# Optimization experiments

Measured on AMD Instinct MI355X. Metric: run time of the kernel, lower is better.

The kernel has to match this reference:

```python
import jax, jax.numpy as jnp
import numpy as np

D_MODEL = 1024
NUM_HEADS = 16
SEQ_LEN = 2048
BATCH = 2
THETA = 10000.0


def apply_rope(x, positions, theta=THETA):
    # x: [b, h, s, d]; positions: [s] int
    d = x.shape[-1]
    inv_freq = 1.0 / (theta ** (jnp.arange(0, d, 2, dtype=jnp.float32) / d))  # [d/2]
    ang = positions.astype(jnp.float32)[:, None] * inv_freq[None, :]  # [s, d/2]
    cos, sin = jnp.cos(ang), jnp.sin(ang)  # [s, d/2]
    x_even = x[..., 0::2]
    x_odd = x[..., 1::2]
    out_even = x_even * cos - x_odd * sin
    out_odd = x_even * sin + x_odd * cos
    # re-interleave pairs
    out = jnp.stack([out_even, out_odd], axis=-1).reshape(x.shape)
    return out


def setup_inputs() -> dict:
    key = jax.random.key(0)
    ks = jax.random.split(key, 5)
    scale = 1.0 / np.sqrt(D_MODEL)
    return {
        "in_features": jax.random.normal(ks[0], (BATCH, SEQ_LEN, D_MODEL), dtype=jnp.float32),
        "token_positions": jnp.arange(SEQ_LEN, dtype=jnp.int32),
        "q_w": jax.random.normal(ks[1], (D_MODEL, D_MODEL), dtype=jnp.float32) * scale,
        "k_w": jax.random.normal(ks[2], (D_MODEL, D_MODEL), dtype=jnp.float32) * scale,
        "v_w": jax.random.normal(ks[3], (D_MODEL, D_MODEL), dtype=jnp.float32) * scale,
        "o_w": jax.random.normal(ks[4], (D_MODEL, D_MODEL), dtype=jnp.float32) * scale,
    }


def reference(in_features, token_positions, q_w, k_w, v_w, o_w):
    b, s, _ = in_features.shape
    h = NUM_HEADS
    d_k = D_MODEL // h

    # Linear stores weights [out, in]: y = x @ W^T
    def proj(x, w):
        y = jnp.einsum('bsi,oi->bso', x, w)
        return y.reshape(b, s, h, d_k).transpose(0, 2, 1, 3)  # [b, h, s, d]

    q = apply_rope(proj(in_features, q_w), token_positions)
    k = apply_rope(proj(in_features, k_w), token_positions)
    v = proj(in_features, v_w)

    scores = jnp.einsum('bhqd,bhkd->bhqk', q, k) / jnp.sqrt(jnp.float32(d_k))
    causal = jnp.tril(jnp.ones((s, s), dtype=bool))
    scores = jnp.where(causal, scores, jnp.float32(-1e30))
    attn = jax.nn.softmax(scores, axis=-1)
    out = jnp.einsum('bhqk,bhkd->bhqd', attn, v)  # [b, h, s, d]
    out = out.transpose(0, 2, 1, 3).reshape(b, s, h * d_k)
    return jnp.einsum('bsi,oi->bso', out, o_w)
```

## Files before the change

kernel.cpp:

```cpp
#include <hip/hip_runtime.h>
#include <hip/hip_bf16.h>

typedef unsigned short ushort_t;
typedef unsigned int uint_t;
typedef __attribute__((ext_vector_type(4))) float f32x4;
typedef __attribute__((ext_vector_type(16))) float f32x16;
typedef __attribute__((ext_vector_type(8))) short short8;
typedef __attribute__((ext_vector_type(4))) short short4x;
typedef __attribute__((ext_vector_type(4))) unsigned short u16x4;
typedef __attribute__((ext_vector_type(2))) uint_t u32x2;

typedef const __attribute__((address_space(1))) unsigned char glob_t;
typedef __attribute__((address_space(3))) unsigned char lds_t;

#define S_LEN 2048
#define DM 1024
#define NH 16
#define DH 64
#define NB 2
#define BH (NB*NH)
#define MROWS (NB*S_LEN)

#define SCALE_L2E 0.18033688f

__device__ __forceinline__ float bf2f(ushort_t u) {
    return __uint_as_float(((uint_t)u) << 16);
}
__device__ __forceinline__ ushort_t f2bf(float f) {
    __hip_bfloat16 h = __float2bfloat16(f);
    return *reinterpret_cast<ushort_t*>(&h);
}

__global__ __launch_bounds__(256) void convert_all(
    const float* __restrict__ X,  const float* __restrict__ Wq,
    const float* __restrict__ Wk, const float* __restrict__ Wv,
    const float* __restrict__ Wo,
    ushort_t* __restrict__ Xb,  ushort_t* __restrict__ Wqb,
    ushort_t* __restrict__ Wkb, ushort_t* __restrict__ Wvb,
    ushort_t* __restrict__ Wob)
{
    size_t i = (size_t)blockIdx.x * 256 + threadIdx.x;
    size_t e = i * 4;
    const float* src; ushort_t* dst; size_t off;
    if (e < (size_t)MROWS * DM) { src = X; dst = Xb; off = e; }
    else {
        size_t r = e - (size_t)MROWS * DM;
        int w = (int)(r >> 20); off = r & 1048575;
        src = (w == 0) ? Wq : (w == 1) ? Wk : (w == 2) ? Wv : Wo;
        dst = (w == 0) ? Wqb : (w == 1) ? Wkb : (w == 2) ? Wvb : Wob;
    }
    float4 v = *reinterpret_cast<const float4*>(src + off);
    u16x4 o;
    o[0] = f2bf(v.x); o[1] = f2bf(v.y); o[2] = f2bf(v.z); o[3] = f2bf(v.w);
    *reinterpret_cast<u16x4*>(dst + off) = o;
}

__global__ __launch_bounds__(256) void rope_table_k(
    const int* __restrict__ pos, float2* __restrict__ tab)
{
    int i = blockIdx.x * 256 + threadIdx.x;
    int s = i >> 5, f = i & 31;
    float inv = powf(10000.0f, -(float)f / 32.0f);
    float ang = (float)pos[s] * inv;
    tab[i] = make_float2(cosf(ang), sinf(ang));
}

template<int MODE>
__global__ __launch_bounds__(256) void gemm128b(
    const ushort_t* __restrict__ A,
    const ushort_t* __restrict__ W0, const ushort_t* __restrict__ W1,
    const ushort_t* __restrict__ W2,
    ushort_t* __restrict__ D0, ushort_t* __restrict__ D1,
    ushort_t* __restrict__ D2,
    float* __restrict__ Fout, const float2* __restrict__ tab)
{
    __shared__ __attribute__((aligned(16))) ushort_t As[128 * 32];
    __shared__ __attribute__((aligned(16))) ushort_t Bs[128 * 32];
    const ushort_t* W = (MODE == 1 || blockIdx.z == 0) ? W0
                        : (blockIdx.z == 1 ? W1 : W2);
    ushort_t* Dst = (blockIdx.z == 0) ? D0 : (blockIdx.z == 1) ? D1 : D2;
    int m0 = blockIdx.x * 128, n0 = blockIdx.y * 128;
    int tid = threadIdx.x, lane = tid & 63, wv = tid >> 6;
    int wm = wv >> 1, wn = wv & 1;
    int l15 = lane & 15, g = lane >> 4;

    f32x4 acc[4][4];
    for (int i = 0; i < 4; i++)
        for (int j = 0; j < 4; j++)
            acc[i][j] = (f32x4){0.f, 0.f, 0.f, 0.f};

    int srow = wv * 32 + (lane >> 2);
    int scol = (lane & 3) * 8;
    const ushort_t* Ap = A + (size_t)(m0 + srow) * DM + scol;
    const ushort_t* Wp = W + (size_t)(n0 + srow) * DM + scol;
    lds_t* laA0 = (lds_t*)&As[wv * 1024];
    lds_t* laA1 = (lds_t*)&As[wv * 1024 + 512];
    lds_t* laB0 = (lds_t*)&Bs[wv * 1024];
    lds_t* laB1 = (lds_t*)&Bs[wv * 1024 + 512];

    for (int kk = 0; kk < DM; kk += 32) {
        __builtin_amdgcn_global_load_lds((glob_t*)(Ap + kk), laA0, 16, 0, 0);
        __builtin_amdgcn_global_load_lds((glob_t*)(Ap + 16 * DM + kk), laA1, 16, 0, 0);
        __builtin_amdgcn_global_load_lds((glob_t*)(Wp + kk), laB0, 16, 0, 0);
        __builtin_amdgcn_global_load_lds((glob_t*)(Wp + 16 * DM + kk), laB1, 16, 0, 0);
        __syncthreads();
        short8 af[4], bf[4];
        for (int i = 0; i < 4; i++)
            af[i] = *reinterpret_cast<const short8*>(
                &As[(wm * 64 + i * 16 + l15) * 32 + g * 8]);
        for (int j = 0; j < 4; j++)
            bf[j] = *reinterpret_cast<const short8*>(
                &Bs[(wn * 64 + j * 16 + l15) * 32 + g * 8]);
        __builtin_amdgcn_s_setprio(1);
        for (int i = 0; i < 4; i++)
            for (int j = 0; j < 4; j++)
                acc[i][j] = __builtin_amdgcn_mfma_f32_16x16x32_bf16(
                    af[i], bf[j], acc[i][j], 0, 0, 0);
        __builtin_amdgcn_s_setprio(0);
        __syncthreads();
    }

    for (int i = 0; i < 4; i++) {
        for (int j = 0; j < 4; j++) {
            int mbase = m0 + wm * 64 + i * 16 + g * 4;
            int n = n0 + wn * 64 + j * 16 + l15;
            if (MODE == 0) {
                int h = n >> 6, d = n & 63;
                if (blockIdx.z < 2) {
                    int f = d >> 1;
                    float sgn = (d & 1) ? 1.f : -1.f;
                    float sc = (blockIdx.z == 0) ? SCALE_L2E : 1.0f;
                    for (int r = 0; r < 4; r++) {
                        int m = mbase + r;
                        int b = m >> 11, s = m & 2047;
                        float v = acc[i][j][r];
                        float p = __shfl_xor(v, 1);
                        float2 cs = tab[s * 32 + f];
                        float out = (v * cs.x + p * cs.y * sgn) * sc;
                        Dst[(((size_t)(b * NH + h)) * S_LEN + s) * DH + d] =
                            f2bf(out);
                    }
                } else {
                    for (int r = 0; r < 4; r++) {
                        int m = mbase + r;
                        int b = m >> 11, s = m & 2047;
                        Dst[((size_t)(b * NH + h) * DH + d) * S_LEN + s] =
                            f2bf(acc[i][j][r]);
                    }
                }
            } else {
                for (int r = 0; r < 4; r++)
                    Fout[(size_t)(mbase + r) * DM + n] = acc[i][j][r];
            }
        }
    }
}

__global__ __launch_bounds__(256, 2) void attn_k6(
    const ushort_t* __restrict__ Q, const ushort_t* __restrict__ K,
    const ushort_t* __restrict__ Vt, ushort_t* __restrict__ O)
{
    __shared__ __attribute__((aligned(16))) ushort_t Ks[2][4096];
    __shared__ __attribute__((aligned(16))) ushort_t Vs[2][4096];

    int tid = threadIdx.x, wv = tid >> 6, lane = tid & 63;
    int l31 = lane & 31, h = lane >> 5, r7 = l31 & 7;
    int bid = blockIdx.x;
    int grp = bid >> 5;
    int u = (bid < 256) ? (15 - grp) : (grp - 8);
    int bh = bid & 31;
    int qb0 = u * 128;
    int qmin = qb0 + wv * 32, qmax = qmin + 31;
    int nt = 2 * u + 2;

    const ushort_t* Qp = Q + (size_t)bh * S_LEN * DH;
    const char* Kp = (const char*)(K + (size_t)bh * S_LEN * DH);
    const char* Vp = (const char*)(Vt + (size_t)bh * DH * S_LEN);

    short8 qf[4];
    {
        const ushort_t* qp = Qp + (((size_t)(qmin + l31)) << 6) + h * 8;
        #pragma unroll
        for (int ds = 0; ds < 4; ds++)
            qf[ds] = *reinterpret_cast<const short8*>(qp + ds * 16);
    }

    f32x16 oacc[2];
    oacc[0] = (f32x16){0.f};
    oacc[1] = (f32x16){0.f};
    float m_run = -INFINITY, l_run = 0.f;

#define STAGE6(buf, kk0) do {                                                 \
    _Pragma("unroll") for (int c_ = 0; c_ < 2; ++c_) {                        \
        int L_ = c_ * 4096 + wv * 1024 + lane * 16;                           \
        int row_ = L_ >> 7;                                                   \
        int col_ = (L_ & 127) ^ ((row_ & 7) << 4);                            \
        __builtin_amdgcn_global_load_lds(                                     \
            (glob_t*)(Kp + (size_t)((kk0) + row_) * 128 + col_),              \
            (lds_t*)((char*)&Ks[buf][0] + c_ * 4096 + wv * 1024), 16, 0, 0);  \
        __builtin_amdgcn_global_load_lds(                                     \
            (glob_t*)(Vp + (size_t)row_ * (S_LEN * 2) + (size_t)(kk0) * 2     \
                      + col_),                                                \
            (lds_t*)((char*)&Vs[buf][0] + c_ * 4096 + wv * 1024), 16, 0, 0);  \
    } } while (0)

    STAGE6(0, 0);
    __syncthreads();

    int cur = 0;
    for (int t = 0; t < nt; ++t) {
        int k0 = t << 6;
        if (t + 1 < nt) STAGE6(cur ^ 1, (t + 1) << 6);

        if (k0 <= qmax) {
            const char* kb = (const char*)&Ks[cur][0];
            const char* vbp = (const char*)&Vs[cur][0];
            short8 kf[2][4];
            #pragma unroll
            for (int s = 0; s < 2; s++)
                #pragma unroll
                for (int ds = 0; ds < 4; ds++)
                    kf[s][ds] = *reinterpret_cast<const short8*>(
                        kb + (s * 32 + l31) * 128 + (((h + 2 * ds) ^ r7) << 4));
            short4x vb[2][2][4];
            #pragma unroll
            for (int ss = 0; ss < 2; ss++)
                #pragma unroll
                for (int db = 0; db < 2; db++)
                    #pragma unroll
                    for (int kt = 0; kt < 4; kt++)
                        vb[ss][db][kt] = *reinterpret_cast<const short4x*>(
                            vbp + (db * 32 + l31) * 128
                            + ((((ss << 2) + kt) ^ r7) << 4) + h * 8);

            f32x16 st[2];
            __builtin_amdgcn_s_setprio(1);
            #pragma unroll
            for (int s = 0; s < 2; s++) {
                f32x16 z = {0.f};
                #pragma unroll
                for (int ds = 0; ds < 4; ds++)
                    z = __builtin_amdgcn_mfma_f32_32x32x16_bf16(
                        kf[s][ds], qf[ds], z, 0, 0, 0);
                st[s] = z;
            }
            __builtin_amdgcn_s_setprio(0);

            if (k0 + 63 > qmin) {
                int q = qmin + l31;
                #pragma unroll
                for (int s = 0; s < 2; s++)
                    #pragma unroll
                    for (int r = 0; r < 16; r++)
                        if ((k0 + s * 32 + (r & 3) + 8 * (r >> 2) + 4 * h) > q)
                            st[s][r] = -1e30f;
            }

            float m0v = fmaxf(st[0][0], st[0][1]);
            #pragma unroll
            for (int r = 2; r < 16; r++) m0v = fmaxf(m0v, st[0][r]);
            float m1v = fmaxf(st[1][0], st[1][1]);
            #pragma unroll
            for (int r = 2; r < 16; r++) m1v = fmaxf(m1v, st[1][r]);
            float m16 = fmaxf(m0v, m1v);
            m16 = fmaxf(m16, __shfl_xor(m16, 32));

            if (!__all(m16 <= m_run + 11.5f)) {
                float m_new = fmaxf(m_run, m16);
                float alpha = exp2f(m_run - m_new);
                m_run = m_new;
                l_run *= alpha;
                oacc[0] *= alpha;
                oacc[1] *= alpha;
            }

            float ps = 0.f;
            short4x pa[2][4];
            #pragma unroll
            for (int s = 0; s < 2; s++)
                #pragma unroll
                for (int kt = 0; kt < 4; kt++) {
                    float p0 = exp2f(st[s][4 * kt + 0] - m_run);
                    float p1 = exp2f(st[s][4 * kt + 1] - m_run);
                    float p2 = exp2f(st[s][4 * kt + 2] - m_run);
                    float p3 = exp2f(st[s][4 * kt + 3] - m_run);
                    ps += (p0 + p1) + (p2 + p3);
                    u32x2 w = { (uint_t)f2bf(p0) | ((uint_t)f2bf(p1) << 16),
                                (uint_t)f2bf(p2) | ((uint_t)f2bf(p3) << 16) };
                    pa[s][kt] = __builtin_bit_cast(short4x, w);
                }
            ps += __shfl_xor(ps, 32);
            l_run += ps;

            __builtin_amdgcn_s_setprio(1);
            #pragma unroll
            for (int s = 0; s < 2; s++)
                #pragma unroll
                for (int kt = 0; kt < 4; kt++) {
                    oacc[0] = __builtin_amdgcn_mfma_f32_32x32x8bf16_1k(
                        vb[s][0][kt], pa[s][kt], oacc[0], 0, 0, 0);
                    oacc[1] = __builtin_amdgcn_mfma_f32_32x32x8bf16_1k(
                        vb[s][1][kt], pa[s][kt], oacc[1], 0, 0, 0);
                }
            __builtin_amdgcn_s_setprio(0);
        }

        __syncthreads();
        cur ^= 1;
    }

    float inv = 1.0f / l_run;
    int b = bh >> 4, head = bh & 15;
    int q_row = qmin + l31;
    size_t obase = ((size_t)b * S_LEN + q_row) * DM + head * DH;
    #pragma unroll
    for (int db = 0; db < 2; db++)
        #pragma unroll
        for (int rg = 0; rg < 4; rg++) {
            u16x4 o;
            #pragma unroll
            for (int j = 0; j < 4; j++)
                o[j] = f2bf(oacc[db][rg * 4 + j] * inv);
            *reinterpret_cast<u16x4*>(&O[obase + db * 32 + rg * 8 + h * 4]) = o;
        }
#undef STAGE6
}

extern "C" void kernel_launch(void* const* d_in, const int* in_sizes, int n_in,
                              void* d_out, int out_size, void* d_ws, size_t ws_size,
                              hipStream_t stream)
{
    const float* X  = (const float*)d_in[0];
    const int* pos  = (const int*)d_in[1];
    const float* qw = (const float*)d_in[2];
    const float* kw = (const float*)d_in[3];
    const float* vw = (const float*)d_in[4];
    const float* ow = (const float*)d_in[5];
    float* out = (float*)d_out;

    char* ws = (char*)d_ws;
    ushort_t* Xb   = (ushort_t*)(ws);
    ushort_t* Wqb  = (ushort_t*)(ws + 8388608);
    ushort_t* Wkb  = (ushort_t*)(ws + 10485760);
    ushort_t* Wvb  = (ushort_t*)(ws + 12582912);
    ushort_t* Wob  = (ushort_t*)(ws + 14680064);
    ushort_t* Qbh  = (ushort_t*)(ws + 16777216);
    ushort_t* Kbh  = (ushort_t*)(ws + 25165824);
    ushort_t* Vtb  = (ushort_t*)(ws + 41943040);
    ushort_t* AttO = (ushort_t*)(ws + 50331648);
    float2*   tab  = (float2*)(ws + 58720256);

    convert_all<<<8192, 256, 0, stream>>>(X, qw, kw, vw, ow,
                                          Xb, Wqb, Wkb, Wvb, Wob);
    rope_table_k<<<256, 256, 0, stream>>>(pos, tab);
    gemm128b<0><<<dim3(32, 8, 3), 256, 0, stream>>>(
        Xb, Wqb, Wkb, Wvb, Qbh, Kbh, Vtb, nullptr, tab);
    attn_k6<<<512, 256, 0, stream>>>(Qbh, Kbh, Vtb, AttO);
    gemm128b<1><<<dim3(32, 8, 1), 256, 0, stream>>>(
        AttO, Wob, nullptr, nullptr, nullptr, nullptr, nullptr, out, tab);
}
```

Before: 144.0 us.

## Split attention into 64-row query blocks with two waves per block

```diff
diff --git a/kernel.cpp b/kernel.cpp
--- a/kernel.cpp
+++ b/kernel.cpp
@@ -156,7 +156,7 @@
     }
 }
 
-__global__ __launch_bounds__(256, 2) void attn_k6(
+__global__ __launch_bounds__(128, 3) void attn_k7(
     const ushort_t* __restrict__ Q, const ushort_t* __restrict__ K,
     const ushort_t* __restrict__ Vt, ushort_t* __restrict__ O)
 {
@@ -166,12 +166,9 @@
     int tid = threadIdx.x, wv = tid >> 6, lane = tid & 63;
     int l31 = lane & 31, h = lane >> 5, r7 = l31 & 7;
     int bid = blockIdx.x;
-    int grp = bid >> 5;
-    int u = (bid < 256) ? (15 - grp) : (grp - 8);
+    int u = 31 - (bid >> 5);
     int bh = bid & 31;
-    int qb0 = u * 128;
-    int qmin = qb0 + wv * 32, qmax = qmin + 31;
-    int nt = 2 * u + 2;
+    int qmin = u * 64 + wv * 32;
 
     const ushort_t* Qp = Q + (size_t)bh * S_LEN * DH;
     const char* Kp = (const char*)(K + (size_t)bh * S_LEN * DH);
@@ -190,120 +187,120 @@
     oacc[1] = (f32x16){0.f};
     float m_run = -INFINITY, l_run = 0.f;
 
-#define STAGE6(buf, kk0) do {                                                 \
-    _Pragma("unroll") for (int c_ = 0; c_ < 2; ++c_) {                        \
-        int L_ = c_ * 4096 + wv * 1024 + lane * 16;                           \
+#define STAGE7(buf, kk0) do {                                                 \
+    _Pragma("unroll") for (int c_ = 0; c_ < 4; ++c_) {                        \
+        int L_ = c_ * 2048 + tid * 16;                                        \
         int row_ = L_ >> 7;                                                   \
         int col_ = (L_ & 127) ^ ((row_ & 7) << 4);                            \
         __builtin_amdgcn_global_load_lds(                                     \
             (glob_t*)(Kp + (size_t)((kk0) + row_) * 128 + col_),              \
-            (lds_t*)((char*)&Ks[buf][0] + c_ * 4096 + wv * 1024), 16, 0, 0);  \
+            (lds_t*)((char*)&Ks[buf][0] + c_ * 2048 + wv * 1024), 16, 0, 0);  \
         __builtin_amdgcn_global_load_lds(                                     \
             (glob_t*)(Vp + (size_t)row_ * (S_LEN * 2) + (size_t)(kk0) * 2     \
                       + col_),                                                \
-            (lds_t*)((char*)&Vs[buf][0] + c_ * 4096 + wv * 1024), 16, 0, 0);  \
+            (lds_t*)((char*)&Vs[buf][0] + c_ * 2048 + wv * 1024), 16, 0, 0);  \
     } } while (0)
 
-    STAGE6(0, 0);
+    STAGE7(0, 0);
     __syncthreads();
 
     int cur = 0;
-    for (int t = 0; t < nt; ++t) {
+    for (int t = 0; t <= u; ++t) {
         int k0 = t << 6;
-        if (t + 1 < nt) STAGE6(cur ^ 1, (t + 1) << 6);
-
-        if (k0 <= qmax) {
-            const char* kb = (const char*)&Ks[cur][0];
-            const char* vbp = (const char*)&Vs[cur][0];
-            short8 kf[2][4];
+        if (t < u) STAGE7(cur ^ 1, (t + 1) << 6);
+
+        const char* kb = (const char*)&Ks[cur][0];
+        const char* vbp = (const char*)&Vs[cur][0];
+        short8 kf[2][4];
+        #pragma unroll
+        for (int s = 0; s < 2; s++)
+            #pragma unroll
+            for (int ds = 0; ds < 4; ds++)
+                kf[s][ds] = *reinterpret_cast<const short8*>(
+                    kb + (s * 32 + l31) * 128 + (((h + 2 * ds) ^ r7) << 4));
+        short4x vb[2][2][4];
+        #pragma unroll
+        for (int ss = 0; ss < 2; ss++)
+            #pragma unroll
+            for (int db = 0; db < 2; db++)
+                #pragma unroll
+                for (int kt = 0; kt < 4; kt++)
+                    vb[ss][db][kt] = *reinterpret_cast<const short4x*>(
+                        vbp + (db * 32 + l31) * 128
+                        + ((((ss << 2) + kt) ^ r7) << 4) + h * 8);
+
+        f32x16 st[2];
+        __builtin_amdgcn_s_setprio(1);
+        #pragma unroll
+        for (int s = 0; s < 2; s++) {
+            f32x16 z = {0.f};
+            #pragma unroll
+            for (int ds = 0; ds < 4; ds++)
+                z = __builtin_amdgcn_mfma_f32_32x32x16_bf16(
+                    kf[s][ds], qf[ds], z, 0, 0, 0);
+            st[s] = z;
+        }
+        __builtin_amdgcn_s_setprio(0);
+
+        if (t == u) {
+            int q = qmin + l31;
             #pragma unroll
             for (int s = 0; s < 2; s++)
                 #pragma unroll
-                for (int ds = 0; ds < 4; ds++)
-                    kf[s][ds] = *reinterpret_cast<const short8*>(
-                        kb + (s * 32 + l31) * 128 + (((h + 2 * ds) ^ r7) << 4));
-            short4x vb[2][2][4];
-            #pragma unroll
-            for (int ss = 0; ss < 2; ss++)
-                #pragma unroll
-                for (int db = 0; db < 2; db++)
-                    #pragma unroll
-                    for (int kt = 0; kt < 4; kt++)
-                        vb[ss][db][kt] = *reinterpret_cast<const short4x*>(
-                            vbp + (db * 32 + l31) * 128
-                            + ((((ss << 2) + kt) ^ r7) << 4) + h * 8);
-
-            f32x16 st[2];
-            __builtin_amdgcn_s_setprio(1);
-            #pragma unroll
-            for (int s = 0; s < 2; s++) {
-                f32x16 z = {0.f};
-                #pragma unroll
-                for (int ds = 0; ds < 4; ds++)
-                    z = __builtin_amdgcn_mfma_f32_32x32x16_bf16(
-                        kf[s][ds], qf[ds], z, 0, 0, 0);
-                st[s] = z;
+                for (int r = 0; r < 16; r++)
+                    if ((k0 + s * 32 + (r & 3) + 8 * (r >> 2) + 4 * h) > q)
+                        st[s][r] = -1e30f;
+        }
+
+        float m0v = st[0][0], m1v = st[1][0];
+        #pragma unroll
+        for (int r = 1; r < 15; r += 2) {
+            m0v = fmaxf(fmaxf(m0v, st[0][r]), st[0][r + 1]);
+            m1v = fmaxf(fmaxf(m1v, st[1][r]), st[1][r + 1]);
+        }
+        m0v = fmaxf(m0v, st[0][15]);
+        m1v = fmaxf(m1v, st[1][15]);
+        float m16 = fmaxf(m0v, m1v);
+        m16 = fmaxf(m16, __shfl_xor(m16, 32));
+
+        if (!__all(m16 <= m_run + 11.5f)) {
+            float m_new = fmaxf(m_run, m16);
+            float alpha = exp2f(m_run - m_new);
+            m_run = m_new;
+            l_run *= alpha;
+            oacc[0] *= alpha;
+            oacc[1] *= alpha;
+        }
+
+        float ps = 0.f;
+        short4x pa[2][4];
+        #pragma unroll
+        for (int s = 0; s < 2; s++)
+            #pragma unroll
+            for (int kt = 0; kt < 4; kt++) {
+                float p0 = exp2f(st[s][4 * kt + 0] - m_run);
+                float p1 = exp2f(st[s][4 * kt + 1] - m_run);
+                float p2 = exp2f(st[s][4 * kt + 2] - m_run);
+                float p3 = exp2f(st[s][4 * kt + 3] - m_run);
+                ps += (p0 + p1) + (p2 + p3);
+                u32x2 w = { (uint_t)f2bf(p0) | ((uint_t)f2bf(p1) << 16),
+                            (uint_t)f2bf(p2) | ((uint_t)f2bf(p3) << 16) };
+                pa[s][kt] = __builtin_bit_cast(short4x, w);
             }
-            __builtin_amdgcn_s_setprio(0);
-
-            if (k0 + 63 > qmin) {
-                int q = qmin + l31;
-                #pragma unroll
-                for (int s = 0; s < 2; s++)
-                    #pragma unroll
-                    for (int r = 0; r < 16; r++)
-                        if ((k0 + s * 32 + (r & 3) + 8 * (r >> 2) + 4 * h) > q)
-                            st[s][r] = -1e30f;
+        ps += __shfl_xor(ps, 32);
+        l_run += ps;
+
+        __builtin_amdgcn_s_setprio(1);
+        #pragma unroll
+        for (int s = 0; s < 2; s++)
+            #pragma unroll
+            for (int kt = 0; kt < 4; kt++) {
+                oacc[0] = __builtin_amdgcn_mfma_f32_32x32x8bf16_1k(
+                    vb[s][0][kt], pa[s][kt], oacc[0], 0, 0, 0);
+                oacc[1] = __builtin_amdgcn_mfma_f32_32x32x8bf16_1k(
+                    vb[s][1][kt], pa[s][kt], oacc[1], 0, 0, 0);
             }
-
-            float m0v = fmaxf(st[0][0], st[0][1]);
-            #pragma unroll
-            for (int r = 2; r < 16; r++) m0v = fmaxf(m0v, st[0][r]);
-            float m1v = fmaxf(st[1][0], st[1][1]);
-            #pragma unroll
-            for (int r = 2; r < 16; r++) m1v = fmaxf(m1v, st[1][r]);
-            float m16 = fmaxf(m0v, m1v);
-            m16 = fmaxf(m16, __shfl_xor(m16, 32));
-
-            if (!__all(m16 <= m_run + 11.5f)) {
-                float m_new = fmaxf(m_run, m16);
-                float alpha = exp2f(m_run - m_new);
-                m_run = m_new;
-                l_run *= alpha;
-                oacc[0] *= alpha;
-                oacc[1] *= alpha;
-            }
-
-            float ps = 0.f;
-            short4x pa[2][4];
-            #pragma unroll
-            for (int s = 0; s < 2; s++)
-                #pragma unroll
-                for (int kt = 0; kt < 4; kt++) {
-                    float p0 = exp2f(st[s][4 * kt + 0] - m_run);
-                    float p1 = exp2f(st[s][4 * kt + 1] - m_run);
-                    float p2 = exp2f(st[s][4 * kt + 2] - m_run);
-                    float p3 = exp2f(st[s][4 * kt + 3] - m_run);
-                    ps += (p0 + p1) + (p2 + p3);
-                    u32x2 w = { (uint_t)f2bf(p0) | ((uint_t)f2bf(p1) << 16),
-                                (uint_t)f2bf(p2) | ((uint_t)f2bf(p3) << 16) };
-                    pa[s][kt] = __builtin_bit_cast(short4x, w);
-                }
-            ps += __shfl_xor(ps, 32);
-            l_run += ps;
-
-            __builtin_amdgcn_s_setprio(1);
-            #pragma unroll
-            for (int s = 0; s < 2; s++)
-                #pragma unroll
-                for (int kt = 0; kt < 4; kt++) {
-                    oacc[0] = __builtin_amdgcn_mfma_f32_32x32x8bf16_1k(
-                        vb[s][0][kt], pa[s][kt], oacc[0], 0, 0, 0);
-                    oacc[1] = __builtin_amdgcn_mfma_f32_32x32x8bf16_1k(
-                        vb[s][1][kt], pa[s][kt], oacc[1], 0, 0, 0);
-                }
-            __builtin_amdgcn_s_setprio(0);
-        }
+        __builtin_amdgcn_s_setprio(0);
 
         __syncthreads();
         cur ^= 1;
@@ -323,7 +320,7 @@
                 o[j] = f2bf(oacc[db][rg * 4 + j] * inv);
             *reinterpret_cast<u16x4*>(&O[obase + db * 32 + rg * 8 + h * 4]) = o;
         }
-#undef STAGE6
+#undef STAGE7
 }
 
 extern "C" void kernel_launch(void* const* d_in, const int* in_sizes, int n_in,
@@ -355,7 +352,7 @@
     rope_table_k<<<256, 256, 0, stream>>>(pos, tab);
     gemm128b<0><<<dim3(32, 8, 3), 256, 0, stream>>>(
         Xb, Wqb, Wkb, Wvb, Qbh, Kbh, Vtb, nullptr, tab);
-    attn_k6<<<512, 256, 0, stream>>>(Qbh, Kbh, Vtb, AttO);
+    attn_k7<<<1024, 128, 0, stream>>>(Qbh, Kbh, Vtb, AttO);
     gemm128b<1><<<dim3(32, 8, 1), 256, 0, stream>>>(
         AttO, Wob, nullptr, nullptr, nullptr, nullptr, nullptr, out, tab);
 }
```

Result: slower. 160.0 us (+11.1%).

## Triple-buffer K/V tiles in attention with vmcnt-based partial waits

Applied to the files above, without the earlier changes.

```diff
diff --git a/kernel.cpp b/kernel.cpp
--- a/kernel.cpp
+++ b/kernel.cpp
@@ -156,12 +156,15 @@
     }
 }
 
-__global__ __launch_bounds__(256, 2) void attn_k6(
+#define WAITV4 asm volatile("s_waitcnt vmcnt(4)" ::: "memory")
+#define WAITV0 asm volatile("s_waitcnt vmcnt(0)" ::: "memory")
+
+__global__ __launch_bounds__(256, 2) void attn_k8(
     const ushort_t* __restrict__ Q, const ushort_t* __restrict__ K,
     const ushort_t* __restrict__ Vt, ushort_t* __restrict__ O)
 {
-    __shared__ __attribute__((aligned(16))) ushort_t Ks[2][4096];
-    __shared__ __attribute__((aligned(16))) ushort_t Vs[2][4096];
+    __shared__ __attribute__((aligned(16))) ushort_t Ks[3][4096];
+    __shared__ __attribute__((aligned(16))) ushort_t Vs[3][4096];
 
     int tid = threadIdx.x, wv = tid >> 6, lane = tid & 63;
     int l31 = lane & 31, h = lane >> 5, r7 = l31 & 7;
@@ -190,7 +193,7 @@
     oacc[1] = (f32x16){0.f};
     float m_run = -INFINITY, l_run = 0.f;
 
-#define STAGE6(buf, kk0) do {                                                 \
+#define STAGE8(buf, kk0) do {                                                 \
     _Pragma("unroll") for (int c_ = 0; c_ < 2; ++c_) {                        \
         int L_ = c_ * 4096 + wv * 1024 + lane * 16;                           \
         int row_ = L_ >> 7;                                                   \
@@ -204,17 +207,21 @@
             (lds_t*)((char*)&Vs[buf][0] + c_ * 4096 + wv * 1024), 16, 0, 0);  \
     } } while (0)
 
-    STAGE6(0, 0);
-    __syncthreads();
-
-    int cur = 0;
+    STAGE8(0, 0);
+    STAGE8(1, 64);
+    WAITV4;
+    __builtin_amdgcn_s_barrier();
+
+    int cs = 0;
     for (int t = 0; t < nt; ++t) {
         int k0 = t << 6;
-        if (t + 1 < nt) STAGE6(cur ^ 1, (t + 1) << 6);
+        int s2 = (cs >= 1) ? cs - 1 : cs + 2;
+        bool willstage = (t + 2 < nt);
+        if (willstage) STAGE8(s2, (t + 2) << 6);
 
         if (k0 <= qmax) {
-            const char* kb = (const char*)&Ks[cur][0];
-            const char* vbp = (const char*)&Vs[cur][0];
+            const char* kb = (const char*)&Ks[cs][0];
+            const char* vbp = (const char*)&Vs[cs][0];
             short8 kf[2][4];
             #pragma unroll
             for (int s = 0; s < 2; s++)
@@ -256,12 +263,14 @@
                             st[s][r] = -1e30f;
             }
 
-            float m0v = fmaxf(st[0][0], st[0][1]);
-            #pragma unroll
-            for (int r = 2; r < 16; r++) m0v = fmaxf(m0v, st[0][r]);
-            float m1v = fmaxf(st[1][0], st[1][1]);
-            #pragma unroll
-            for (int r = 2; r < 16; r++) m1v = fmaxf(m1v, st[1][r]);
+            float m0v = st[0][0], m1v = st[1][0];
+            #pragma unroll
+            for (int r = 1; r < 15; r += 2) {
+                m0v = fmaxf(fmaxf(m0v, st[0][r]), st[0][r + 1]);
+                m1v = fmaxf(fmaxf(m1v, st[1][r]), st[1][r + 1]);
+            }
+            m0v = fmaxf(m0v, st[0][15]);
+            m1v = fmaxf(m1v, st[1][15]);
             float m16 = fmaxf(m0v, m1v);
             m16 = fmaxf(m16, __shfl_xor(m16, 32));
 
@@ -305,8 +314,9 @@
             __builtin_amdgcn_s_setprio(0);
         }
 
-        __syncthreads();
-        cur ^= 1;
+        if (willstage) { WAITV4; } else { WAITV0; }
+        __builtin_amdgcn_s_barrier();
+        cs = (cs >= 2) ? 0 : cs + 1;
     }
 
     float inv = 1.0f / l_run;
@@ -323,7 +333,7 @@
                 o[j] = f2bf(oacc[db][rg * 4 + j] * inv);
             *reinterpret_cast<u16x4*>(&O[obase + db * 32 + rg * 8 + h * 4]) = o;
         }
-#undef STAGE6
+#undef STAGE8
 }
 
 extern "C" void kernel_launch(void* const* d_in, const int* in_sizes, int n_in,
@@ -355,7 +365,7 @@
     rope_table_k<<<256, 256, 0, stream>>>(pos, tab);
     gemm128b<0><<<dim3(32, 8, 3), 256, 0, stream>>>(
         Xb, Wqb, Wkb, Wvb, Qbh, Kbh, Vtb, nullptr, tab);
-    attn_k6<<<512, 256, 0, stream>>>(Qbh, Kbh, Vtb, AttO);
+    attn_k8<<<512, 256, 0, stream>>>(Qbh, Kbh, Vtb, AttO);
     gemm128b<1><<<dim3(32, 8, 1), 256, 0, stream>>>(
         AttO, Wob, nullptr, nullptr, nullptr, nullptr, nullptr, out, tab);
 }
```

After: 145.1 us. Within noise of the previous version (+0.8%).
